# Kernel optimization log

Measured on AMD Instinct MI355X. Metric: run time of the kernel, lower is better.

The kernel has to match this reference:

```python
import jax, jax.numpy as jnp
import numpy as np

N_S, N_T, E = 50000, 50000, 600000
D_IN, D_H, D_OUT = 256, 128, 64


def setup_inputs() -> dict:
    key = jax.random.key(0)
    k1, k2, k3, k4, k5, k6 = jax.random.split(key, 6)
    edge_src = jax.random.randint(k1, (E,), 0, N_S, dtype=jnp.int32)
    edge_dst = jax.random.randint(k2, (E,), 0, N_T, dtype=jnp.int32)
    edge_index = jnp.stack([edge_src, edge_dst], axis=0)  # [2, E]
    x_s = jax.random.normal(k3, (N_S, D_IN), dtype=jnp.float32)
    x_t = jax.random.normal(k4, (N_T, D_IN), dtype=jnp.float32)
    W0 = jax.random.normal(k5, (D_IN, D_H), dtype=jnp.float32) * (1.0 / np.sqrt(D_IN))
    W1 = jax.random.normal(k6, (D_H, D_OUT), dtype=jnp.float32) * (1.0 / np.sqrt(D_H))
    return {"edge_index": edge_index, "x_s": x_s, "x_t": x_t, "W0": W0, "W1": W1}


def gcn_conv(x, src, dst, W):
    """PyG GCNConv, bias=False: D^{-1/2}(A+I)D^{-1/2} (x @ W)."""
    N = x.shape[0]
    h = x @ W  # [N, out]
    loops = jnp.arange(N, dtype=src.dtype)
    s = jnp.concatenate([src, loops])  # add self-loops
    d = jnp.concatenate([dst, loops])
    deg = jax.ops.segment_sum(jnp.ones_like(d, dtype=h.dtype), d, num_segments=N)
    dinv = jnp.where(deg > 0, jax.lax.rsqrt(deg), 0.0)
    norm = dinv[s] * dinv[d]  # [E+N]
    return jax.ops.segment_sum(h[s] * norm[:, None], d, num_segments=N)


def reference(edge_index, x_s, x_t, W0, W1):
    n_s = x_s.shape[0]
    src = edge_index[0]
    dst = edge_index[1] + n_s  # targets live in the x_t block
    acts = [jax.nn.relu, lambda v: v]
    Ws = [W0, W1]
    for W, act in zip(Ws, acts):
        x = jnp.concatenate([x_s, x_t], axis=0)
        x = act(gcn_conv(x, src, dst, W))
        x_s, x_t = x[:n_s], x[n_s:]
    return (x_s, x_t)
```

## Files before the change

### kernel.cpp

```cpp
#include <hip/hip_runtime.h>
#include <cstdint>
#include <cstddef>

typedef unsigned short u16;
typedef unsigned int   u32;
typedef __attribute__((ext_vector_type(8))) short bf16x8;
typedef __attribute__((ext_vector_type(4))) float f32x4;

#define D_IN  256
#define D_H   128
#define D_OUT 64
#define LSTR  72

__device__ __forceinline__ float bf2f(u16 u){
  union { u32 i; float f; } v; v.i = ((u32)u) << 16; return v.f;
}
__device__ __forceinline__ u16 f2bf(float f){
  union { float f; u32 i; } v; v.f = f;
  u32 r = (v.i + 0x7fffu + ((v.i >> 16) & 1u)) >> 16;
  return (u16)r;
}

__global__ void k_zero(int* __restrict__ p, int n){
  int i = blockIdx.x * 256 + threadIdx.x;
  if (i < n) p[i] = 0;
}

__global__ void k_deg(const int* __restrict__ dst, int E, int* __restrict__ deg){
  int e = blockIdx.x * 256 + threadIdx.x;
  if (e < E) atomicAdd(&deg[dst[e]], 1);
}

__global__ __launch_bounds__(256) void k_bsum(const int* __restrict__ deg, int N,
                                              int* __restrict__ bsum){
  __shared__ int s[256];
  int tid = threadIdx.x;
  int i = blockIdx.x * 256 + tid;
  s[tid] = (i < N) ? deg[i] : 0;
  __syncthreads();
  for (int o = 128; o > 0; o >>= 1){
    if (tid < o) s[tid] += s[tid + o];
    __syncthreads();
  }
  if (tid == 0) bsum[blockIdx.x] = s[0];
}

__global__ __launch_bounds__(256) void k_bscan(int* __restrict__ bsum, int nb){
  __shared__ int s[256];
  int tid = threadIdx.x;
  int v = (tid < nb) ? bsum[tid] : 0;
  s[tid] = v;
  __syncthreads();
  for (int o = 1; o < 256; o <<= 1){
    int t = (tid >= o) ? s[tid - o] : 0;
    __syncthreads();
    s[tid] += t;
    __syncthreads();
  }
  if (tid < nb) bsum[tid] = s[tid] - v;
}

__global__ __launch_bounds__(256) void k_off(const int* __restrict__ deg, int N,
                                             const int* __restrict__ bsum,
                                             int* __restrict__ off, int* __restrict__ cursor,
                                             float* __restrict__ dinv){
  __shared__ int s[256];
  int tid = threadIdx.x;
  int i = blockIdx.x * 256 + tid;
  int v = (i < N) ? deg[i] : 0;
  s[tid] = v;
  __syncthreads();
  for (int o = 1; o < 256; o <<= 1){
    int t = (tid >= o) ? s[tid - o] : 0;
    __syncthreads();
    s[tid] += t;
    __syncthreads();
  }
  if (i < N){
    int excl = s[tid] - v + bsum[blockIdx.x];
    off[i] = excl;
    cursor[i] = excl;
    dinv[i] = rsqrtf((float)v + 1.0f);
  }
}

__global__ void k_fill(const int* __restrict__ src, const int* __restrict__ dst,
                       int E, int* __restrict__ cursor, int* __restrict__ csr){
  int e = blockIdx.x * 256 + threadIdx.x;
  if (e < E){
    int d = dst[e];
    int p = atomicAdd(&cursor[d], 1);
    csr[p] = src[e];
  }
}

__global__ void k_wprep(const float* __restrict__ W0, const float* __restrict__ W1,
                        u16* __restrict__ W0t, u16* __restrict__ W1t){
  int i = blockIdx.x * 256 + threadIdx.x;
  if (i < 128 * 256){
    int n = i >> 8, k = i & 255;
    W0t[i] = f2bf(W0[(size_t)k * 128 + n]);
  } else if (i < 128 * 256 + 64 * 128){
    int j = i - 128 * 256;
    int n = j >> 7, k = j & 127;
    W1t[j] = f2bf(W1[(size_t)k * 64 + n]);
  }
}

__global__ __launch_bounds__(256) void k_gemm1(
    const float* __restrict__ Xs, const float* __restrict__ Xt,
    const u16* __restrict__ W0t, int M, int n_s,
    u16* __restrict__ out)
{
  __shared__ u16 As[128 * LSTR];
  __shared__ u16 Bs[128 * LSTR];
  const int t    = threadIdx.x;
  const int wave = t >> 6, lane = t & 63;
  const int wm   = (wave >> 1) * 64, wn = (wave & 1) * 64;
  const int lm   = lane & 15, quad = lane >> 4;
  const int row0 = blockIdx.x * 128;

  f32x4 acc[4][4];
  const f32x4 z = {0.f, 0.f, 0.f, 0.f};
  #pragma unroll
  for (int i = 0; i < 4; i++)
    #pragma unroll
    for (int j = 0; j < 4; j++) acc[i][j] = z;

  const int ar = t >> 1;
  const int kh = (t & 1) * 32;
  const int r  = row0 + ar;
  const float* xp = nullptr;
  if (r < M) xp = (r < n_s) ? (Xs + (size_t)r * D_IN) : (Xt + (size_t)(r - n_s) * D_IN);
  const u16* wrow = W0t + (size_t)ar * D_IN + kh;

  for (int k0 = 0; k0 < D_IN; k0 += 64){
    u16 abuf[32];
    if (xp){
      #pragma unroll
      for (int j = 0; j < 8; j++){
        float4 v = *(const float4*)(xp + k0 + kh + j * 4);
        abuf[j*4+0] = f2bf(v.x); abuf[j*4+1] = f2bf(v.y);
        abuf[j*4+2] = f2bf(v.z); abuf[j*4+3] = f2bf(v.w);
      }
    } else {
      #pragma unroll
      for (int j = 0; j < 32; j++) abuf[j] = 0;
    }
    int4 b0 = *(const int4*)(wrow + k0);
    int4 b1 = *(const int4*)(wrow + k0 + 8);
    int4 b2 = *(const int4*)(wrow + k0 + 16);
    int4 b3 = *(const int4*)(wrow + k0 + 24);

    __syncthreads();
    {
      u16* ap = &As[ar * LSTR + kh];
      *(int4*)(ap +  0) = *(int4*)&abuf[0];
      *(int4*)(ap +  8) = *(int4*)&abuf[8];
      *(int4*)(ap + 16) = *(int4*)&abuf[16];
      *(int4*)(ap + 24) = *(int4*)&abuf[24];
      u16* bp = &Bs[ar * LSTR + kh];
      *(int4*)(bp +  0) = b0;
      *(int4*)(bp +  8) = b1;
      *(int4*)(bp + 16) = b2;
      *(int4*)(bp + 24) = b3;
    }
    __syncthreads();

    #pragma unroll
    for (int kk = 0; kk < 64; kk += 32){
      bf16x8 af[4], bf[4];
      #pragma unroll
      for (int i = 0; i < 4; i++)
        af[i] = *(const bf16x8*)&As[(wm + i*16 + lm) * LSTR + kk + quad*8];
      #pragma unroll
      for (int i = 0; i < 4; i++)
        bf[i] = *(const bf16x8*)&Bs[(wn + i*16 + lm) * LSTR + kk + quad*8];
      #pragma unroll
      for (int mi = 0; mi < 4; mi++)
        #pragma unroll
        for (int ni = 0; ni < 4; ni++)
          acc[mi][ni] = __builtin_amdgcn_mfma_f32_16x16x32_bf16(
              af[mi], bf[ni], acc[mi][ni], 0, 0, 0);
    }
  }

  #pragma unroll
  for (int mi = 0; mi < 4; mi++){
    int rbase = row0 + wm + mi * 16 + quad * 4;
    #pragma unroll
    for (int rr = 0; rr < 4; rr++){
      int m = rbase + rr;
      if (m >= M) continue;
      u16* op = out + (size_t)m * D_H + wn + lm;
      #pragma unroll
      for (int ni = 0; ni < 4; ni++)
        op[ni * 16] = f2bf(acc[mi][ni][rr]);
    }
  }
}

__global__ __launch_bounds__(256) void k_gemm2(
    const u16* __restrict__ h1, const u16* __restrict__ W1t,
    int M, float* __restrict__ out)
{
  __shared__ u16 As[128 * LSTR];
  __shared__ u16 Bs[64 * LSTR];
  const int t    = threadIdx.x;
  const int wave = t >> 6, lane = t & 63;
  const int wm   = wave * 32;
  const int lm   = lane & 15, quad = lane >> 4;
  const int row0 = blockIdx.x * 128;

  f32x4 acc[2][4];
  const f32x4 z = {0.f, 0.f, 0.f, 0.f};
  #pragma unroll
  for (int i = 0; i < 2; i++)
    #pragma unroll
    for (int j = 0; j < 4; j++) acc[i][j] = z;

  const int ar = t >> 1;
  const int kh = (t & 1) * 32;
  const int r  = row0 + ar;
  const int bn = t >> 2;
  const int bk = (t & 3) * 16;

  for (int k0 = 0; k0 < D_H; k0 += 64){
    u16 abuf[32];
    if (r < M){
      const u16* hp = h1 + (size_t)r * D_H + k0 + kh;
      #pragma unroll
      for (int j = 0; j < 4; j++){
        int4 v = *(const int4*)(hp + j * 8);
        u16* hh = (u16*)&v;
        #pragma unroll
        for (int q = 0; q < 8; q++)
          abuf[j*8+q] = (hh[q] & 0x8000u) ? (u16)0 : hh[q];
      }
    } else {
      #pragma unroll
      for (int j = 0; j < 32; j++) abuf[j] = 0;
    }
    int4 w0 = *(const int4*)(W1t + (size_t)bn * D_H + k0 + bk);
    int4 w1 = *(const int4*)(W1t + (size_t)bn * D_H + k0 + bk + 8);

    __syncthreads();
    {
      u16* ap = &As[ar * LSTR + kh];
      *(int4*)(ap +  0) = *(int4*)&abuf[0];
      *(int4*)(ap +  8) = *(int4*)&abuf[8];
      *(int4*)(ap + 16) = *(int4*)&abuf[16];
      *(int4*)(ap + 24) = *(int4*)&abuf[24];
      u16* bp = &Bs[bn * LSTR + bk];
      *(int4*)(bp + 0) = w0;
      *(int4*)(bp + 8) = w1;
    }
    __syncthreads();

    #pragma unroll
    for (int kk = 0; kk < 64; kk += 32){
      bf16x8 af[2], bf[4];
      #pragma unroll
      for (int i = 0; i < 2; i++)
        af[i] = *(const bf16x8*)&As[(wm + i*16 + lm) * LSTR + kk + quad*8];
      #pragma unroll
      for (int i = 0; i < 4; i++)
        bf[i] = *(const bf16x8*)&Bs[(i*16 + lm) * LSTR + kk + quad*8];
      #pragma unroll
      for (int mi = 0; mi < 2; mi++)
        #pragma unroll
        for (int ni = 0; ni < 4; ni++)
          acc[mi][ni] = __builtin_amdgcn_mfma_f32_16x16x32_bf16(
              af[mi], bf[ni], acc[mi][ni], 0, 0, 0);
    }
  }

  #pragma unroll
  for (int mi = 0; mi < 2; mi++){
    int rbase = row0 + wm + mi * 16 + quad * 4;
    #pragma unroll
    for (int rr = 0; rr < 4; rr++){
      int m = rbase + rr;
      if (m >= M) continue;
      float* op = out + (size_t)m * D_OUT + lm;
      #pragma unroll
      for (int ni = 0; ni < 4; ni++)
        op[ni * 16] = acc[mi][ni][rr];
    }
  }
}

__global__ __launch_bounds__(256) void k_agg1(
    const int* __restrict__ off, const int* __restrict__ deg,
    const int* __restrict__ csr, const float* __restrict__ dinv,
    u16* __restrict__ h1, int n_s, int n_t)
{
  int w    = (blockIdx.x * 256 + threadIdx.x) >> 6;
  int lane = threadIdx.x & 63;
  if (w >= n_t) return;
  int start = off[w];
  int n     = deg[w];

  float s0 = 0.f, s1 = 0.f, s2 = 0.f, s3 = 0.f;
  int i = 0;
  for (; i + 2 <= n; i += 2){
    int sa = csr[start + i];
    int sb = csr[start + i + 1];
    u32 da = *(const u32*)(h1 + (size_t)sa * D_H + lane * 2);
    u32 db = *(const u32*)(h1 + (size_t)sb * D_H + lane * 2);
    s0 += bf2f((u16)da); s1 += bf2f((u16)(da >> 16));
    s2 += bf2f((u16)db); s3 += bf2f((u16)(db >> 16));
  }
  if (i < n){
    int sa = csr[start + i];
    u32 da = *(const u32*)(h1 + (size_t)sa * D_H + lane * 2);
    s0 += bf2f((u16)da); s1 += bf2f((u16)(da >> 16));
  }
  s0 += s2; s1 += s3;

  float di  = dinv[w];
  float di2 = di * di;
  u32* selfp = (u32*)(h1 + (size_t)(n_s + w) * D_H + lane * 2);
  u32 ht = *selfp;
  float v0 = fmaxf(di * s0 + di2 * bf2f((u16)ht), 0.f);
  float v1 = fmaxf(di * s1 + di2 * bf2f((u16)(ht >> 16)), 0.f);
  *selfp = (u32)f2bf(v0) | ((u32)f2bf(v1) << 16);
}

__global__ __launch_bounds__(256) void k_agg2(
    const int* __restrict__ off, const int* __restrict__ deg,
    const int* __restrict__ csr, const float* __restrict__ dinv,
    float* __restrict__ y, int n_s, int n_t)
{
  int w    = (blockIdx.x * 256 + threadIdx.x) >> 6;
  int lane = threadIdx.x & 63;
  if (w >= n_t) return;
  int start = off[w];
  int n     = deg[w];

  float s0 = 0.f, s1 = 0.f;
  int i = 0;
  for (; i + 2 <= n; i += 2){
    int sa = csr[start + i];
    int sb = csr[start + i + 1];
    s0 += y[(size_t)sa * D_OUT + lane];
    s1 += y[(size_t)sb * D_OUT + lane];
  }
  if (i < n){
    int sa = csr[start + i];
    s0 += y[(size_t)sa * D_OUT + lane];
  }
  s0 += s1;

  float di = dinv[w];
  float* selfp = y + (size_t)(n_s + w) * D_OUT + lane;
  *selfp = di * s0 + di * di * (*selfp);
}

static inline size_t alup(size_t x){ return (x + 255) & ~(size_t)255; }

extern "C" void kernel_launch(void* const* d_in, const int* in_sizes, int n_in,
                              void* d_out, int out_size, void* d_ws, size_t ws_size,
                              hipStream_t stream)
{
  const int*   ei = (const int*)d_in[0];
  const float* xs = (const float*)d_in[1];
  const float* xt = (const float*)d_in[2];
  const float* W0 = (const float*)d_in[3];
  const float* W1 = (const float*)d_in[4];
  const int E   = in_sizes[0] / 2;
  const int n_s = in_sizes[1] / D_IN;
  const int n_t = in_sizes[2] / D_IN;
  const int M   = n_s + n_t;
  const int* src = ei;
  const int* dst = ei + E;
  const int nb_t = (n_t + 255) / 256;

  char* p = (char*)d_ws;
  int*   deg    = (int*)p;    p += alup((size_t)n_t * 4);
  int*   off    = (int*)p;    p += alup((size_t)n_t * 4);
  int*   cursor = (int*)p;    p += alup((size_t)n_t * 4);
  float* dinv   = (float*)p;  p += alup((size_t)n_t * 4);
  int*   bsum   = (int*)p;    p += alup((size_t)nb_t * 4);
  int*   csr    = (int*)p;    p += alup((size_t)E * 4);
  u16*   W0t    = (u16*)p;    p += alup((size_t)D_H * D_IN * 2);
  u16*   W1t    = (u16*)p;    p += alup((size_t)D_OUT * D_H * 2);
  u16*   h1     = (u16*)p;    p += alup((size_t)M * D_H * 2);

  k_wprep <<<(128*256 + 64*128 + 255) / 256, 256, 0, stream>>>(W0, W1, W0t, W1t);
  k_zero  <<<nb_t, 256, 0, stream>>>(deg, n_t);
  k_deg   <<<(E + 255) / 256, 256, 0, stream>>>(dst, E, deg);
  k_bsum  <<<nb_t, 256, 0, stream>>>(deg, n_t, bsum);
  k_bscan <<<1, 256, 0, stream>>>(bsum, nb_t);
  k_off   <<<nb_t, 256, 0, stream>>>(deg, n_t, bsum, off, cursor, dinv);
  k_fill  <<<(E + 255) / 256, 256, 0, stream>>>(src, dst, E, cursor, csr);

  k_gemm1<<<(M + 127) / 128, 256, 0, stream>>>(xs, xt, W0t, M, n_s, h1);
  k_agg1<<<(n_t + 3) / 4, 256, 0, stream>>>(off, deg, csr, dinv, h1, n_s, n_t);

  k_gemm2<<<(M + 127) / 128, 256, 0, stream>>>(h1, W1t, M, (float*)d_out);
  k_agg2<<<(n_t + 3) / 4, 256, 0, stream>>>(off, deg, csr, dinv,
                                            (float*)d_out, n_s, n_t);
}
```

Before: 310.6 us.

## Fuse both aggregations before second GEMM via linearity; prefetch GEMM tiles

Because the second layer's aggregation is linear, it is applied before the W1 GEMM instead of after it. A single aggregation kernel computes the layer-1 output and also the layer-2 aggregate of ReLU'd source features, which removes one gather pass and one kernel launch. k_gemm2 then applies ReLU only to source rows. Both GEMMs now register-prefetch the next K tile while MFMAs run, and the deg zeroing is folded into the weight-prep kernel. The aggregated rows are rounded to bf16 before the W1 multiply, which changes rounding relative to the previous ordering.

Result: faster. 285.0 us (-8.2%).

```diff
diff --git a/kernel.cpp b/kernel.cpp
--- a/kernel.cpp
+++ b/kernel.cpp
@@ -21,9 +21,20 @@
   return (u16)r;
 }
 
-__global__ void k_zero(int* __restrict__ p, int n){
+__global__ void k_wprep(const float* __restrict__ W0, const float* __restrict__ W1,
+                        u16* __restrict__ W0t, u16* __restrict__ W1t,
+                        int* __restrict__ deg, int n_t){
   int i = blockIdx.x * 256 + threadIdx.x;
-  if (i < n) p[i] = 0;
+  if (i < 128 * 256){
+    int n = i >> 8, k = i & 255;
+    W0t[i] = f2bf(W0[(size_t)k * 128 + n]);
+  } else if (i < 128 * 256 + 64 * 128){
+    int j = i - 128 * 256;
+    int n = j >> 7, k = j & 127;
+    W1t[j] = f2bf(W1[(size_t)k * 64 + n]);
+  } else if (i - (128 * 256 + 64 * 128) < n_t){
+    deg[i - (128 * 256 + 64 * 128)] = 0;
+  }
 }
 
 __global__ void k_deg(const int* __restrict__ dst, int E, int* __restrict__ deg){
@@ -94,19 +105,6 @@
   }
 }
 
-__global__ void k_wprep(const float* __restrict__ W0, const float* __restrict__ W1,
-                        u16* __restrict__ W0t, u16* __restrict__ W1t){
-  int i = blockIdx.x * 256 + threadIdx.x;
-  if (i < 128 * 256){
-    int n = i >> 8, k = i & 255;
-    W0t[i] = f2bf(W0[(size_t)k * 128 + n]);
-  } else if (i < 128 * 256 + 64 * 128){
-    int j = i - 128 * 256;
-    int n = j >> 7, k = j & 127;
-    W1t[j] = f2bf(W1[(size_t)k * 64 + n]);
-  }
-}
-
 __global__ __launch_bounds__(256) void k_gemm1(
     const float* __restrict__ Xs, const float* __restrict__ Xt,
     const u16* __restrict__ W0t, int M, int n_s,
@@ -134,54 +132,65 @@
   if (r < M) xp = (r < n_s) ? (Xs + (size_t)r * D_IN) : (Xt + (size_t)(r - n_s) * D_IN);
   const u16* wrow = W0t + (size_t)ar * D_IN + kh;
 
+  float4 a4[8];
+  int4   b4[4];
+  if (xp){
+    #pragma unroll
+    for (int j = 0; j < 8; j++) a4[j] = *(const float4*)(xp + kh + j * 4);
+  } else {
+    float4 zz = make_float4(0,0,0,0);
+    #pragma unroll
+    for (int j = 0; j < 8; j++) a4[j] = zz;
+  }
+  #pragma unroll
+  for (int j = 0; j < 4; j++) b4[j] = *(const int4*)(wrow + j * 8);
+
   for (int k0 = 0; k0 < D_IN; k0 += 64){
-    u16 abuf[32];
-    if (xp){
+    __syncthreads();
+    {
+      u16 abuf[32];
       #pragma unroll
       for (int j = 0; j < 8; j++){
-        float4 v = *(const float4*)(xp + k0 + kh + j * 4);
-        abuf[j*4+0] = f2bf(v.x); abuf[j*4+1] = f2bf(v.y);
-        abuf[j*4+2] = f2bf(v.z); abuf[j*4+3] = f2bf(v.w);
+        abuf[j*4+0] = f2bf(a4[j].x); abuf[j*4+1] = f2bf(a4[j].y);
+        abuf[j*4+2] = f2bf(a4[j].z); abuf[j*4+3] = f2bf(a4[j].w);
       }
-    } else {
-      #pragma unroll
-      for (int j = 0; j < 32; j++) abuf[j] = 0;
-    }
-    int4 b0 = *(const int4*)(wrow + k0);
-    int4 b1 = *(const int4*)(wrow + k0 + 8);
-    int4 b2 = *(const int4*)(wrow + k0 + 16);
-    int4 b3 = *(const int4*)(wrow + k0 + 24);
-
-    __syncthreads();
-    {
       u16* ap = &As[ar * LSTR + kh];
       *(int4*)(ap +  0) = *(int4*)&abuf[0];
       *(int4*)(ap +  8) = *(int4*)&abuf[8];
       *(int4*)(ap + 16) = *(int4*)&abuf[16];
       *(int4*)(ap + 24) = *(int4*)&abuf[24];
       u16* bp = &Bs[ar * LSTR + kh];
-      *(int4*)(bp +  0) = b0;
-      *(int4*)(bp +  8) = b1;
-      *(int4*)(bp + 16) = b2;
-      *(int4*)(bp + 24) = b3;
-    }
-    __syncthreads();
+      *(int4*)(bp +  0) = b4[0];
+      *(int4*)(bp +  8) = b4[1];
+      *(int4*)(bp + 16) = b4[2];
+      *(int4*)(bp + 24) = b4[3];
+    }
+    __syncthreads();
+
+    if (k0 + 64 < D_IN){
+      if (xp){
+        #pragma unroll
+        for (int j = 0; j < 8; j++) a4[j] = *(const float4*)(xp + k0 + 64 + kh + j * 4);
+      }
+      #pragma unroll
+      for (int j = 0; j < 4; j++) b4[j] = *(const int4*)(wrow + k0 + 64 + j * 8);
+    }
 
     #pragma unroll
     for (int kk = 0; kk < 64; kk += 32){
-      bf16x8 af[4], bf[4];
+      bf16x8 af[4], bfr[4];
       #pragma unroll
       for (int i = 0; i < 4; i++)
         af[i] = *(const bf16x8*)&As[(wm + i*16 + lm) * LSTR + kk + quad*8];
       #pragma unroll
       for (int i = 0; i < 4; i++)
-        bf[i] = *(const bf16x8*)&Bs[(wn + i*16 + lm) * LSTR + kk + quad*8];
+        bfr[i] = *(const bf16x8*)&Bs[(wn + i*16 + lm) * LSTR + kk + quad*8];
       #pragma unroll
       for (int mi = 0; mi < 4; mi++)
         #pragma unroll
         for (int ni = 0; ni < 4; ni++)
           acc[mi][ni] = __builtin_amdgcn_mfma_f32_16x16x32_bf16(
-              af[mi], bf[ni], acc[mi][ni], 0, 0, 0);
+              af[mi], bfr[ni], acc[mi][ni], 0, 0, 0);
     }
   }
 
@@ -200,97 +209,7 @@
   }
 }
 
-__global__ __launch_bounds__(256) void k_gemm2(
-    const u16* __restrict__ h1, const u16* __restrict__ W1t,
-    int M, float* __restrict__ out)
-{
-  __shared__ u16 As[128 * LSTR];
-  __shared__ u16 Bs[64 * LSTR];
-  const int t    = threadIdx.x;
-  const int wave = t >> 6, lane = t & 63;
-  const int wm   = wave * 32;
-  const int lm   = lane & 15, quad = lane >> 4;
-  const int row0 = blockIdx.x * 128;
-
-  f32x4 acc[2][4];
-  const f32x4 z = {0.f, 0.f, 0.f, 0.f};
-  #pragma unroll
-  for (int i = 0; i < 2; i++)
-    #pragma unroll
-    for (int j = 0; j < 4; j++) acc[i][j] = z;
-
-  const int ar = t >> 1;
-  const int kh = (t & 1) * 32;
-  const int r  = row0 + ar;
-  const int bn = t >> 2;
-  const int bk = (t & 3) * 16;
-
-  for (int k0 = 0; k0 < D_H; k0 += 64){
-    u16 abuf[32];
-    if (r < M){
-      const u16* hp = h1 + (size_t)r * D_H + k0 + kh;
-      #pragma unroll
-      for (int j = 0; j < 4; j++){
-        int4 v = *(const int4*)(hp + j * 8);
-        u16* hh = (u16*)&v;
-        #pragma unroll
-        for (int q = 0; q < 8; q++)
-          abuf[j*8+q] = (hh[q] & 0x8000u) ? (u16)0 : hh[q];
-      }
-    } else {
-      #pragma unroll
-      for (int j = 0; j < 32; j++) abuf[j] = 0;
-    }
-    int4 w0 = *(const int4*)(W1t + (size_t)bn * D_H + k0 + bk);
-    int4 w1 = *(const int4*)(W1t + (size_t)bn * D_H + k0 + bk + 8);
-
-    __syncthreads();
-    {
-      u16* ap = &As[ar * LSTR + kh];
-      *(int4*)(ap +  0) = *(int4*)&abuf[0];
-      *(int4*)(ap +  8) = *(int4*)&abuf[8];
-      *(int4*)(ap + 16) = *(int4*)&abuf[16];
-      *(int4*)(ap + 24) = *(int4*)&abuf[24];
-      u16* bp = &Bs[bn * LSTR + bk];
-      *(int4*)(bp + 0) = w0;
-      *(int4*)(bp + 8) = w1;
-    }
-    __syncthreads();
-
-    #pragma unroll
-    for (int kk = 0; kk < 64; kk += 32){
-      bf16x8 af[2], bf[4];
-      #pragma unroll
-      for (int i = 0; i < 2; i++)
-        af[i] = *(const bf16x8*)&As[(wm + i*16 + lm) * LSTR + kk + quad*8];
-      #pragma unroll
-      for (int i = 0; i < 4; i++)
-        bf[i] = *(const bf16x8*)&Bs[(i*16 + lm) * LSTR + kk + quad*8];
-      #pragma unroll
-      for (int mi = 0; mi < 2; mi++)
-        #pragma unroll
-        for (int ni = 0; ni < 4; ni++)
-          acc[mi][ni] = __builtin_amdgcn_mfma_f32_16x16x32_bf16(
-              af[mi], bf[ni], acc[mi][ni], 0, 0, 0);
-    }
-  }
-
-  #pragma unroll
-  for (int mi = 0; mi < 2; mi++){
-    int rbase = row0 + wm + mi * 16 + quad * 4;
-    #pragma unroll
-    for (int rr = 0; rr < 4; rr++){
-      int m = rbase + rr;
-      if (m >= M) continue;
-      float* op = out + (size_t)m * D_OUT + lm;
-      #pragma unroll
-      for (int ni = 0; ni < 4; ni++)
-        op[ni * 16] = acc[mi][ni][rr];
-    }
-  }
-}
-
-__global__ __launch_bounds__(256) void k_agg1(
+__global__ __launch_bounds__(256) void k_aggf(
     const int* __restrict__ off, const int* __restrict__ deg,
     const int* __restrict__ csr, const float* __restrict__ dinv,
     u16* __restrict__ h1, int n_s, int n_t)
@@ -301,60 +220,149 @@
   int start = off[w];
   int n     = deg[w];
 
-  float s0 = 0.f, s1 = 0.f, s2 = 0.f, s3 = 0.f;
+  float r0 = 0.f, r1 = 0.f, p0 = 0.f, p1 = 0.f;
   int i = 0;
-  for (; i + 2 <= n; i += 2){
+  for (; i + 4 <= n; i += 4){
     int sa = csr[start + i];
     int sb = csr[start + i + 1];
+    int sc = csr[start + i + 2];
+    int sd = csr[start + i + 3];
     u32 da = *(const u32*)(h1 + (size_t)sa * D_H + lane * 2);
     u32 db = *(const u32*)(h1 + (size_t)sb * D_H + lane * 2);
-    s0 += bf2f((u16)da); s1 += bf2f((u16)(da >> 16));
-    s2 += bf2f((u16)db); s3 += bf2f((u16)(db >> 16));
-  }
-  if (i < n){
+    u32 dc = *(const u32*)(h1 + (size_t)sc * D_H + lane * 2);
+    u32 dd = *(const u32*)(h1 + (size_t)sd * D_H + lane * 2);
+    float va0 = bf2f((u16)da), va1 = bf2f((u16)(da >> 16));
+    float vb0 = bf2f((u16)db), vb1 = bf2f((u16)(db >> 16));
+    float vc0 = bf2f((u16)dc), vc1 = bf2f((u16)(dc >> 16));
+    float vd0 = bf2f((u16)dd), vd1 = bf2f((u16)(dd >> 16));
+    r0 += va0 + vb0 + vc0 + vd0;
+    r1 += va1 + vb1 + vc1 + vd1;
+    p0 += fmaxf(va0,0.f) + fmaxf(vb0,0.f) + fmaxf(vc0,0.f) + fmaxf(vd0,0.f);
+    p1 += fmaxf(va1,0.f) + fmaxf(vb1,0.f) + fmaxf(vc1,0.f) + fmaxf(vd1,0.f);
+  }
+  for (; i < n; i++){
     int sa = csr[start + i];
     u32 da = *(const u32*)(h1 + (size_t)sa * D_H + lane * 2);
-    s0 += bf2f((u16)da); s1 += bf2f((u16)(da >> 16));
-  }
-  s0 += s2; s1 += s3;
+    float va0 = bf2f((u16)da), va1 = bf2f((u16)(da >> 16));
+    r0 += va0; r1 += va1;
+    p0 += fmaxf(va0,0.f); p1 += fmaxf(va1,0.f);
+  }
 
   float di  = dinv[w];
   float di2 = di * di;
   u32* selfp = (u32*)(h1 + (size_t)(n_s + w) * D_H + lane * 2);
   u32 ht = *selfp;
-  float v0 = fmaxf(di * s0 + di2 * bf2f((u16)ht), 0.f);
-  float v1 = fmaxf(di * s1 + di2 * bf2f((u16)(ht >> 16)), 0.f);
-  *selfp = (u32)f2bf(v0) | ((u32)f2bf(v1) << 16);
-}
-
-__global__ __launch_bounds__(256) void k_agg2(
-    const int* __restrict__ off, const int* __restrict__ deg,
-    const int* __restrict__ csr, const float* __restrict__ dinv,
-    float* __restrict__ y, int n_s, int n_t)
+  float z0 = fmaxf(di * r0 + di2 * bf2f((u16)ht), 0.f);
+  float z1 = fmaxf(di * r1 + di2 * bf2f((u16)(ht >> 16)), 0.f);
+  float u0 = di * p0 + di2 * z0;
+  float u1 = di * p1 + di2 * z1;
+  *selfp = (u32)f2bf(u0) | ((u32)f2bf(u1) << 16);
+}
+
+__global__ __launch_bounds__(256) void k_gemm2(
+    const u16* __restrict__ h1, const u16* __restrict__ W1t,
+    int M, int n_s, float* __restrict__ out)
 {
-  int w    = (blockIdx.x * 256 + threadIdx.x) >> 6;
-  int lane = threadIdx.x & 63;
-  if (w >= n_t) return;
-  int start = off[w];
-  int n     = deg[w];
-
-  float s0 = 0.f, s1 = 0.f;
-  int i = 0;
-  for (; i + 2 <= n; i += 2){
-    int sa = csr[start + i];
-    int sb = csr[start + i + 1];
-    s0 += y[(size_t)sa * D_OUT + lane];
-    s1 += y[(size_t)sb * D_OUT + lane];
-  }
-  if (i < n){
-    int sa = csr[start + i];
-    s0 += y[(size_t)sa * D_OUT + lane];
-  }
-  s0 += s1;
-
-  float di = dinv[w];
-  float* selfp = y + (size_t)(n_s + w) * D_OUT + lane;
-  *selfp = di * s0 + di * di * (*selfp);
+  __shared__ u16 As[128 * LSTR];
+  __shared__ u16 Bs[64 * LSTR];
+  const int t    = threadIdx.x;
+  const int wave = t >> 6, lane = t & 63;
+  const int wm   = wave * 32;
+  const int lm   = lane & 15, quad = lane >> 4;
+  const int row0 = blockIdx.x * 128;
+
+  f32x4 acc[2][4];
+  const f32x4 z = {0.f, 0.f, 0.f, 0.f};
+  #pragma unroll
+  for (int i = 0; i < 2; i++)
+    #pragma unroll
+    for (int j = 0; j < 4; j++) acc[i][j] = z;
+
+  const int ar = t >> 1;
+  const int kh = (t & 1) * 32;
+  const int r  = row0 + ar;
+  const bool relu_a = (r < n_s);
+  const int bn = t >> 2;
+  const int bk = (t & 3) * 16;
+
+  int4 a4[4], w4[2];
+  if (r < M){
+    const u16* hp = h1 + (size_t)r * D_H + kh;
+    #pragma unroll
+    for (int j = 0; j < 4; j++) a4[j] = *(const int4*)(hp + j * 8);
+  } else {
+    int4 zz = make_int4(0,0,0,0);
+    #pragma unroll
+    for (int j = 0; j < 4; j++) a4[j] = zz;
+  }
+  w4[0] = *(const int4*)(W1t + (size_t)bn * D_H + bk);
+  w4[1] = *(const int4*)(W1t + (size_t)bn * D_H + bk + 8);
+
+  for (int k0 = 0; k0 < D_H; k0 += 64){
+    __syncthreads();
+    {
+      u16 abuf[32];
+      #pragma unroll
+      for (int j = 0; j < 4; j++){
+        u16* hh = (u16*)&a4[j];
+        #pragma unroll
+        for (int q = 0; q < 8; q++){
+          u16 v = hh[q];
+          abuf[j*8+q] = (relu_a && (v & 0x8000u)) ? (u16)0 : v;
+        }
+      }
+      u16* ap = &As[ar * LSTR + kh];
+      *(int4*)(ap +  0) = *(int4*)&abuf[0];
+      *(int4*)(ap +  8) = *(int4*)&abuf[8];
+      *(int4*)(ap + 16) = *(int4*)&abuf[16];
+      *(int4*)(ap + 24) = *(int4*)&abuf[24];
+      u16* bp = &Bs[bn * LSTR + bk];
+      *(int4*)(bp + 0) = w4[0];
+      *(int4*)(bp + 8) = w4[1];
+    }
+    __syncthreads();
+
+    if (k0 + 64 < D_H){
+      if (r < M){
+        const u16* hp = h1 + (size_t)r * D_H + k0 + 64 + kh;
+        #pragma unroll
+        for (int j = 0; j < 4; j++) a4[j] = *(const int4*)(hp + j * 8);
+      }
+      w4[0] = *(const int4*)(W1t + (size_t)bn * D_H + k0 + 64 + bk);
+      w4[1] = *(const int4*)(W1t + (size_t)bn * D_H + k0 + 64 + bk + 8);
+    }
+
+    #pragma unroll
+    for (int kk = 0; kk < 64; kk += 32){
+      bf16x8 af[2], bfr[4];
+      #pragma unroll
+      for (int i = 0; i < 2; i++)
+        af[i] = *(const bf16x8*)&As[(wm + i*16 + lm) * LSTR + kk + quad*8];
+      #pragma unroll
+      for (int i = 0; i < 4; i++)
+        bfr[i] = *(const bf16x8*)&Bs[(i*16 + lm) * LSTR + kk + quad*8];
+      #pragma unroll
+      for (int mi = 0; mi < 2; mi++)
+        #pragma unroll
+        for (int ni = 0; ni < 4; ni++)
+          acc[mi][ni] = __builtin_amdgcn_mfma_f32_16x16x32_bf16(
+              af[mi], bfr[ni], acc[mi][ni], 0, 0, 0);
+    }
+  }
+
+  #pragma unroll
+  for (int mi = 0; mi < 2; mi++){
+    int rbase = row0 + wm + mi * 16 + quad * 4;
+    #pragma unroll
+    for (int rr = 0; rr < 4; rr++){
+      int m = rbase + rr;
+      if (m >= M) continue;
+      float* op = out + (size_t)m * D_OUT + lm;
+      #pragma unroll
+      for (int ni = 0; ni < 4; ni++)
+        op[ni * 16] = acc[mi][ni][rr];
+    }
+  }
 }
 
 static inline size_t alup(size_t x){ return (x + 255) & ~(size_t)255; }
@@ -387,8 +395,8 @@
   u16*   W1t    = (u16*)p;    p += alup((size_t)D_OUT * D_H * 2);
   u16*   h1     = (u16*)p;    p += alup((size_t)M * D_H * 2);
 
-  k_wprep <<<(128*256 + 64*128 + 255) / 256, 256, 0, stream>>>(W0, W1, W0t, W1t);
-  k_zero  <<<nb_t, 256, 0, stream>>>(deg, n_t);
+  const int wprep_n = 128*256 + 64*128 + n_t;
+  k_wprep <<<(wprep_n + 255) / 256, 256, 0, stream>>>(W0, W1, W0t, W1t, deg, n_t);
   k_deg   <<<(E + 255) / 256, 256, 0, stream>>>(dst, E, deg);
   k_bsum  <<<nb_t, 256, 0, stream>>>(deg, n_t, bsum);
   k_bscan <<<1, 256, 0, stream>>>(bsum, nb_t);
@@ -396,9 +404,6 @@
   k_fill  <<<(E + 255) / 256, 256, 0, stream>>>(src, dst, E, cursor, csr);
 
   k_gemm1<<<(M + 127) / 128, 256, 0, stream>>>(xs, xt, W0t, M, n_s, h1);
-  k_agg1<<<(n_t + 3) / 4, 256, 0, stream>>>(off, deg, csr, dinv, h1, n_s, n_t);
-
-  k_gemm2<<<(M + 127) / 128, 256, 0, stream>>>(h1, W1t, M, (float*)d_out);
-  k_agg2<<<(n_t + 3) / 4, 256, 0, stream>>>(off, deg, csr, dinv,
-                                            (float*)d_out, n_s, n_t);
-}
+  k_aggf <<<(n_t + 3) / 4, 256, 0, stream>>>(off, deg, csr, dinv, h1, n_s, n_t);
+  k_gemm2<<<(M + 127) / 128, 256, 0, stream>>>(h1, W1t, M, n_s, (float*)d_out);
+}
```
